# Performance work log

Measured on AMD Instinct MI355X. Metric: run time of the kernel, lower is better.

The kernel has to match this reference:

```python
import jax, jax.numpy as jnp
import numpy as np

MD = 4  # max displacement -> (2*MD+1)**2 = 81 shift channels


def setup_inputs() -> dict:
    key = jax.random.key(0)
    k1, k2 = jax.random.split(key)
    B, C, H, W = 4, 64, 192, 320
    tenFirst = jax.random.normal(k1, (B, C, H, W), dtype=jnp.float32)
    tenSecond = jax.random.normal(k2, (B, C, H, W), dtype=jnp.float32)
    return {"tenFirst": tenFirst, "tenSecond": tenSecond}


def reference(tenFirst, tenSecond):
    # Windowed cross-correlation cost volume (PWC-Net style):
    # out[b, k, y, x] = mean_c first[b,c,y,x] * second[b,c,y+dy,x+dx]
    # for (dy,dx) in [-4,4]^2, k = (dy+4)*9 + (dx+4). Out-of-bounds -> 0 via padding.
    B, C, H, W = tenFirst.shape
    padded = jnp.pad(tenSecond, ((0, 0), (0, 0), (MD, MD), (MD, MD)))
    outs = []
    for dy in range(2 * MD + 1):  # fixed small set of 81 shifts
        for dx in range(2 * MD + 1):
            shifted = padded[:, :, dy:dy + H, dx:dx + W]  # [B,C,H,W]
            outs.append(jnp.mean(tenFirst * shifted, axis=1))  # [B,H,W]
    return jnp.stack(outs, axis=1)  # [B,81,H,W]
```

## Files before the change

### kernel.cpp

```cpp
#include <hip/hip_runtime.h>
#include <hip/hip_bf16.h>


#define WW   320
#define HH   192
#define CC   64
#define HWSZ (HH * WW)
#define NB   4
#define PW   328
#define PH   200
#define NDISP 81
#define ESTV 20

typedef __attribute__((ext_vector_type(8))) short bf16x8_t;
typedef __attribute__((ext_vector_type(4))) float f32x4_t;

static __device__ __forceinline__ unsigned short f2bf(float f) {
    unsigned int u = __float_as_uint(f);
    u += 0x7fffu + ((u >> 16) & 1u);
    return (unsigned short)(u >> 16);
}

static __device__ __forceinline__ unsigned pack2(float a, float b) {
    return (unsigned)f2bf(a) | ((unsigned)f2bf(b) << 16);
}

__global__ __launch_bounds__(256, 6)
void conv_s(const float* __restrict__ S,
            unsigned short* __restrict__ Sp) {
    __shared__ float ta[64][65];
    const int t  = threadIdx.x;
    const int x0 = blockIdx.x * 64;
    const int y  = blockIdx.y;
    const int b  = blockIdx.z;

    const int blk = (b * HH + y) * (WW / 64) + blockIdx.x;
    const int gid = blk * 256 + t;
    if (gid < NB * 4160 * 8) {
        int bb = gid / (4160 * 8);
        int r  = gid % (4160 * 8);
        int px = r >> 3;
        int v  = r & 7;
        int row, colp;
        if (px < 2624) {
            int strip = px / 1312;
            int pp    = px % 1312;
            row  = (strip ? 196 : 0) + pp / 328;
            colp = pp % 328;
        } else {
            int tt2 = px - 2624;
            row  = 4 + (tt2 >> 3);
            int tt = tt2 & 7;
            colp = (tt < 4) ? tt : (320 + tt);
        }
        uint4 z; z.x = 0u; z.y = 0u; z.z = 0u; z.w = 0u;
        *(uint4*)((unsigned short*)Sp + ((((size_t)bb * PH + row) * PW + colp) * 8 + v) * 8) = z;
    }

    const int x4 = t & 15;
    const int c0 = t >> 4;
    const float* ssrc = S + (size_t)b * CC * HWSZ + (size_t)y * WW + x0 + 4 * x4;
    float4 vS[4];
#pragma unroll
    for (int k = 0; k < 4; ++k)
        vS[k] = *(const float4*)(ssrc + (size_t)(c0 + 16 * k) * HWSZ);

#pragma unroll
    for (int k = 0; k < 4; ++k) {
        int c = c0 + 16 * k;
        ta[c][4 * x4 + 0] = vS[k].x;
        ta[c][4 * x4 + 1] = vS[k].y;
        ta[c][4 * x4 + 2] = vS[k].z;
        ta[c][4 * x4 + 3] = vS[k].w;
    }
    __syncthreads();

    const int xx = t >> 2;
    const int cg = (t & 3) * 16;
    unsigned short* dst = Sp + (((size_t)b * PH + (y + 4)) * PW + (x0 + xx + 4)) * CC + cg;
    uint4 w;
    w.x = pack2(ta[cg + 0][xx],  ta[cg + 1][xx]);
    w.y = pack2(ta[cg + 2][xx],  ta[cg + 3][xx]);
    w.z = pack2(ta[cg + 4][xx],  ta[cg + 5][xx]);
    w.w = pack2(ta[cg + 6][xx],  ta[cg + 7][xx]);
    *(uint4*)dst = w;
    w.x = pack2(ta[cg + 8][xx],  ta[cg + 9][xx]);
    w.y = pack2(ta[cg + 10][xx], ta[cg + 11][xx]);
    w.z = pack2(ta[cg + 12][xx], ta[cg + 13][xx]);
    w.w = pack2(ta[cg + 14][xx], ta[cg + 15][xx]);
    *(uint4*)(dst + 8) = w;
}

__global__ __launch_bounds__(256, 4)
void corr_mfma_v5(const float* __restrict__ F,
                  const unsigned short* __restrict__ Sp,
                  float* __restrict__ out) {
    __shared__ float ebuf[4][27 * ESTV];

    const int tid  = threadIdx.x;
    const int wave = tid >> 6;
    const int lane = tid & 63;
    const int q    = lane >> 4;
    const int col  = lane & 15;

    const int i    = blockIdx.x;
    const int xcd  = i & 7;
    const int j    = i >> 3;
    const int b    = j / 60;
    const int r60  = j % 60;
    const int pql  = r60 / 20;
    const int xt   = r60 % 20;
    const int pq   = xcd * 3 + pql;
    const int yp   = pq * 4 + wave;
    const int y0   = yp * 2;
    const int x0   = xt * 16;

    const float* fb = F + (size_t)b * CC * HWSZ + (size_t)y0 * WW + x0 + col;
    bf16x8_t a00, a01, a10, a11;
#pragma unroll
    for (int jj = 0; jj < 8; ++jj) {
        a00[jj] = (short)f2bf(fb[(size_t)(q * 8 + jj) * HWSZ]);
        a01[jj] = (short)f2bf(fb[(size_t)(32 + q * 8 + jj) * HWSZ]);
        a10[jj] = (short)f2bf(fb[(size_t)(q * 8 + jj) * HWSZ + WW]);
        a11[jj] = (short)f2bf(fb[(size_t)(32 + q * 8 + jj) * HWSZ + WW]);
    }

    const float scale = 1.0f / 64.0f;
    float* my = ebuf[wave];

    for (int g = 0; g < 3; ++g) {
        const int d0 = g * 3;

        f32x4_t acc[2][3][2];
#pragma unroll
        for (int p = 0; p < 2; ++p)
#pragma unroll
            for (int d = 0; d < 3; ++d)
#pragma unroll
                for (int nt = 0; nt < 2; ++nt)
#pragma unroll
                    for (int k = 0; k < 4; ++k) acc[p][d][nt][k] = 0.f;

#pragma unroll
        for (int rr = 0; rr < 4; ++rr) {
            const unsigned short* srow = Sp + ((size_t)b * PH + (y0 + d0 + rr)) * PW * CC;
#pragma unroll
            for (int nt = 0; nt < 2; ++nt) {
                int xp = x0 + col + 16 * nt;
                xp = xp > (PW - 1) ? (PW - 1) : xp;
                const unsigned short* p = srow + (size_t)xp * CC + q * 8;
                const bf16x8_t b0 = *(const bf16x8_t*)(p);
                const bf16x8_t b1 = *(const bf16x8_t*)(p + 32);
                if (rr < 3) {
                    acc[0][rr][nt] = __builtin_amdgcn_mfma_f32_16x16x32_bf16(a00, b0, acc[0][rr][nt], 0, 0, 0);
                    acc[0][rr][nt] = __builtin_amdgcn_mfma_f32_16x16x32_bf16(a01, b1, acc[0][rr][nt], 0, 0, 0);
                }
                if (rr >= 1) {
                    acc[1][rr - 1][nt] = __builtin_amdgcn_mfma_f32_16x16x32_bf16(a10, b0, acc[1][rr - 1][nt], 0, 0, 0);
                    acc[1][rr - 1][nt] = __builtin_amdgcn_mfma_f32_16x16x32_bf16(a11, b1, acc[1][rr - 1][nt], 0, 0, 0);
                }
            }
        }

#pragma unroll
        for (int p = 0; p < 2; ++p) {
#pragma unroll
            for (int dyi = 0; dyi < 3; ++dyi)
#pragma unroll
                for (int nt = 0; nt < 2; ++nt)
#pragma unroll
                    for (int k = 0; k < 4; ++k) {
                        int m  = 4 * q + k;
                        int dx = col + 16 * nt - m;
                        if (dx >= 0 && dx <= 8)
                            my[(dyi * 9 + dx) * ESTV + m] = acc[p][dyi][nt][k] * scale;
                    }
            float* ob = out + ((size_t)b * NDISP + d0 * 9) * HWSZ + (size_t)(y0 + p) * WW + x0;
#pragma unroll
            for (int rnd = 0; rnd < 2; ++rnd) {
                int idx = rnd * 64 + lane;
                if (idx < 108) {
                    int d  = idx >> 2;
                    int m4 = (idx & 3) * 4;
                    *(float4*)(ob + (size_t)d * HWSZ + m4) = *(const float4*)(my + d * ESTV + m4);
                }
            }
        }
    }
}

#define MDV      4
#define TILE_X   64
#define TILE_Y   8
#define CH_STAGE 4
#define LDS_ROWS (TILE_Y + 2 * MDV)
#define LDS_COLS (TILE_X + 2 * MDV)

__global__ __launch_bounds__(256, 2)
void corr_direct(const float* __restrict__ first,
                 const float* __restrict__ second,
                 float* __restrict__ out) {
    const int C = 64, H = HH, W = WW;
    const int HW = H * W;
    __shared__ float lds[CH_STAGE][LDS_ROWS * LDS_COLS];
    const int tx = threadIdx.x, ty = threadIdx.y;
    const int tid = ty * 32 + tx;
    const int x_tile = blockIdx.x * TILE_X;
    const int y_tile = blockIdx.y * TILE_Y;
    const int b = blockIdx.z;
    const int x0 = x_tile + 2 * tx;
    const int y  = y_tile + ty;
    const float* fst_b = first  + (size_t)b * C * HW;
    const float* sec_b = second + (size_t)b * C * HW;
    float acc[NDISP][2];
#pragma unroll
    for (int d = 0; d < NDISP; ++d) { acc[d][0] = 0.f; acc[d][1] = 0.f; }
    for (int cb = 0; cb < C; cb += CH_STAGE) {
        __syncthreads();
        const int total = CH_STAGE * LDS_ROWS * LDS_COLS;
#pragma unroll
        for (int k = 0; k < total / 256; ++k) {
            int i = tid + k * 256;
            int c   = i / (LDS_ROWS * LDS_COLS);
            int rem = i - c * (LDS_ROWS * LDS_COLS);
            int r   = rem / LDS_COLS;
            int cl  = rem - r * LDS_COLS;
            int gy = y_tile - MDV + r;
            int gx = x_tile - MDV + cl;
            float v = 0.f;
            if ((unsigned)gy < (unsigned)H && (unsigned)gx < (unsigned)W)
                v = sec_b[(size_t)(cb + c) * HW + gy * W + gx];
            lds[c][rem] = v;
        }
        __syncthreads();
#pragma unroll
        for (int cl = 0; cl < CH_STAGE; ++cl) {
            const int c = cb + cl;
            const float2 f = *(const float2*)&fst_b[(size_t)c * HW + y * W + x0];
#pragma unroll
            for (int r = 0; r < 9; ++r) {
                const float* row = &lds[cl][(ty + r) * LDS_COLS + 2 * tx];
                float w[10];
#pragma unroll
                for (int k = 0; k < 5; ++k) {
                    float2 t2 = *(const float2*)&row[2 * k];
                    w[2 * k] = t2.x; w[2 * k + 1] = t2.y;
                }
#pragma unroll
                for (int dx = 0; dx < 9; ++dx) {
                    acc[r * 9 + dx][0] += f.x * w[dx];
                    acc[r * 9 + dx][1] += f.y * w[dx + 1];
                }
            }
        }
    }
    const float scale = 1.0f / 64.0f;
    float* out_b = out + (size_t)b * NDISP * HW;
#pragma unroll
    for (int d = 0; d < NDISP; ++d) {
        float2 o;
        o.x = acc[d][0] * scale;
        o.y = acc[d][1] * scale;
        *(float2*)&out_b[(size_t)d * HW + y * W + x0] = o;
    }
}

extern "C" void kernel_launch(void* const* d_in, const int* in_sizes, int n_in,
                              void* d_out, int out_size, void* d_ws, size_t ws_size,
                              hipStream_t stream) {
    const float* tenFirst  = (const float*)d_in[0];
    const float* tenSecond = (const float*)d_in[1];
    float* out = (float*)d_out;

    const size_t sp_bytes = (size_t)NB * PH * PW * CC * 2;

    if (ws_size >= sp_bytes) {
        unsigned short* Sp = (unsigned short*)d_ws;
        conv_s<<<dim3(WW / 64, HH, NB), 256, 0, stream>>>(tenSecond, Sp);
        corr_mfma_v5<<<1920, 256, 0, stream>>>(tenFirst, Sp, out);
    } else {
        corr_direct<<<dim3(WW / TILE_X, HH / TILE_Y, NB), dim3(32, 8), 0, stream>>>(
            tenFirst, tenSecond, out);
    }
}
```

Baseline: 229.9 us.

## Stage shifted second-image rows in LDS shared across four waves

Each block now covers a 64-pixel-wide strip, with its four waves handling adjacent 16-pixel x-tiles instead of separate row pairs. The four padded Sp rows (80 pixels wide) for each dy-group are loaded cooperatively into XOR-swizzled shared memory, and the MFMA B-operands are read from LDS. The goal is to cut redundant global/L2 traffic from overlapping windows. The cost is about 40KB of LDS, two block barriers per group and a lower occupancy bound.

```diff
diff --git a/kernel.cpp b/kernel.cpp
--- a/kernel.cpp
+++ b/kernel.cpp
@@ -11,6 +11,7 @@
 #define PH   200
 #define NDISP 81
 #define ESTV 20
+#define QWPX 80
 
 typedef __attribute__((ext_vector_type(8))) short bf16x8_t;
 typedef __attribute__((ext_vector_type(4))) float f32x4_t;
@@ -91,15 +92,16 @@
     *(uint4*)(dst + 8) = w;
 }
 
-__global__ __launch_bounds__(256, 4)
-void corr_mfma_v5(const float* __restrict__ F,
+__global__ __launch_bounds__(256, 3)
+void corr_mfma_v6(const float* __restrict__ F,
                   const unsigned short* __restrict__ Sp,
                   float* __restrict__ out) {
+    __shared__ unsigned short sbuf[4 * QWPX * CC];
     __shared__ float ebuf[4][27 * ESTV];
 
-    const int tid  = threadIdx.x;
-    const int wave = tid >> 6;
-    const int lane = tid & 63;
+    const int t    = threadIdx.x;
+    const int wave = t >> 6;
+    const int lane = t & 63;
     const int q    = lane >> 4;
     const int col  = lane & 15;
 
@@ -108,12 +110,12 @@
     const int j    = i >> 3;
     const int b    = j / 60;
     const int r60  = j % 60;
-    const int pql  = r60 / 20;
-    const int xt   = r60 % 20;
-    const int pq   = xcd * 3 + pql;
-    const int yp   = pq * 4 + wave;
+    const int ypl  = r60 / 5;
+    const int quad = r60 % 5;
+    const int yp   = xcd * 12 + ypl;
     const int y0   = yp * 2;
-    const int x0   = xt * 16;
+    const int x0b  = quad * 64;
+    const int x0   = x0b + wave * 16;
 
     const float* fb = F + (size_t)b * CC * HWSZ + (size_t)y0 * WW + x0 + col;
     bf16x8_t a00, a01, a10, a11;
@@ -127,10 +129,28 @@
 
     const float scale = 1.0f / 64.0f;
     float* my = ebuf[wave];
+    const unsigned short* spb = Sp + (size_t)b * PH * PW * CC;
 
     for (int g = 0; g < 3; ++g) {
         const int d0 = g * 3;
 
+#pragma unroll
+        for (int k = 0; k < 10; ++k) {
+            int idx   = t + 256 * k;
+            int chunk = idx & 7;
+            int pxl   = idx >> 3;
+            int rr    = pxl / QWPX;
+            int px    = pxl % QWPX;
+            int xp    = x0b + px;
+            xp = xp > (PW - 1) ? (PW - 1) : xp;
+            const unsigned short* src =
+                spb + ((size_t)(y0 + d0 + rr) * PW + xp) * CC + chunk * 8;
+            bf16x8_t v = *(const bf16x8_t*)src;
+            int lofs = ((pxl * 128) + chunk * 16) ^ ((px & 7) << 4);
+            *(bf16x8_t*)((char*)sbuf + lofs) = v;
+        }
+        __syncthreads();
+
         f32x4_t acc[2][3][2];
 #pragma unroll
         for (int p = 0; p < 2; ++p)
@@ -143,14 +163,12 @@
 
 #pragma unroll
         for (int rr = 0; rr < 4; ++rr) {
-            const unsigned short* srow = Sp + ((size_t)b * PH + (y0 + d0 + rr)) * PW * CC;
 #pragma unroll
             for (int nt = 0; nt < 2; ++nt) {
-                int xp = x0 + col + 16 * nt;
-                xp = xp > (PW - 1) ? (PW - 1) : xp;
-                const unsigned short* p = srow + (size_t)xp * CC + q * 8;
-                const bf16x8_t b0 = *(const bf16x8_t*)(p);
-                const bf16x8_t b1 = *(const bf16x8_t*)(p + 32);
+                int px   = wave * 16 + col + 16 * nt;
+                int base = ((rr * QWPX + px) * 128) ^ ((px & 7) << 4);
+                const bf16x8_t b0 = *(const bf16x8_t*)((char*)sbuf + (base ^ (q * 16)));
+                const bf16x8_t b1 = *(const bf16x8_t*)((char*)sbuf + (base ^ ((q + 4) * 16)));
                 if (rr < 3) {
                     acc[0][rr][nt] = __builtin_amdgcn_mfma_f32_16x16x32_bf16(a00, b0, acc[0][rr][nt], 0, 0, 0);
                     acc[0][rr][nt] = __builtin_amdgcn_mfma_f32_16x16x32_bf16(a01, b1, acc[0][rr][nt], 0, 0, 0);
@@ -161,6 +179,7 @@
                 }
             }
         }
+        __syncthreads();
 
 #pragma unroll
         for (int p = 0; p < 2; ++p) {
@@ -277,7 +296,7 @@
     if (ws_size >= sp_bytes) {
         unsigned short* Sp = (unsigned short*)d_ws;
         conv_s<<<dim3(WW / 64, HH, NB), 256, 0, stream>>>(tenSecond, Sp);
-        corr_mfma_v5<<<1920, 256, 0, stream>>>(tenFirst, Sp, out);
+        corr_mfma_v6<<<1920, 256, 0, stream>>>(tenFirst, Sp, out);
     } else {
         corr_direct<<<dim3(WW / TILE_X, HH / TILE_Y, NB), dim3(32, 8), 0, stream>>>(
             tenFirst, tenSecond, out);
```

Result: faster. 201.2 us (-12.5%).
